# Optimization experiments

Hardware: AMD Instinct MI355X
Metric: run time of the kernel (lower is better)

The kernel has to match this reference:

```python
import jax, jax.numpy as jnp
import numpy as np

N_NODES = 50000
N_EDGES = 800000
N_FEAT = 128
D_HID = 128
N_CLASS = 40


def gcn_conv(x, W, b, src, dst, n_nodes):
    """PyG GCNConv: h = D^{-1/2} (A + I) D^{-1/2} (x @ W) + b.
    src/dst are int arrays [E]; self-loops handled analytically."""
    h = x @ W  # [N, D]
    ones = jnp.ones(src.shape[0], dtype=h.dtype)
    # degree after adding self-loops: 1 + in-degree (edge weights are 1)
    deg = 1.0 + jax.ops.segment_sum(ones, dst, num_segments=n_nodes)
    dinv = jax.lax.rsqrt(deg)  # [N]
    # messages along edges src -> dst with symmetric normalization
    msg = h[src] * (dinv[src] * dinv[dst])[:, None]  # [E, D]
    agg = jax.ops.segment_sum(msg, dst, num_segments=n_nodes)  # [N, D]
    # self-loop contribution: dinv[i]^2 * h[i]
    agg = agg + h * (dinv * dinv)[:, None]
    return agg + b


def setup_inputs() -> dict:
    key = jax.random.key(0)
    ks = jax.random.split(key, 5)
    x = jax.random.normal(ks[0], (N_NODES, N_FEAT), dtype=jnp.float32)
    edge_index = jax.random.randint(ks[1], (2, N_EDGES), 0, N_NODES, dtype=jnp.int64)
    s_in = 1.0 / np.sqrt(N_FEAT)
    s_h = 1.0 / np.sqrt(D_HID)
    W_in = jax.random.normal(ks[2], (N_FEAT, D_HID), dtype=jnp.float32) * s_in
    W1 = jax.random.normal(ks[3], (D_HID, D_HID), dtype=jnp.float32) * s_h
    W_out = jax.random.normal(ks[4], (D_HID, N_CLASS), dtype=jnp.float32) * s_h
    return {
        "x": x,
        "edge_index": edge_index,
        "W_in": W_in,
        "b_in": jnp.zeros((D_HID,), jnp.float32),
        "W1": W1,
        "b1": jnp.zeros((D_HID,), jnp.float32),
        "W_out": W_out,
        "b_out": jnp.zeros((N_CLASS,), jnp.float32),
    }


def reference(x, edge_index, W_in, b_in, W1, b1, W_out, b_out):
    src, dst = edge_index[0], edge_index[1]
    n = x.shape[0]
    # input GCNConv (no activation on input_fc, matching the torch forward)
    h = gcn_conv(x, W_in, b_in, src, dst, n)
    # hidden layer: dropout is identity at eval; relu after conv; normalize=False
    h = jax.nn.relu(gcn_conv(h, W1, b1, src, dst, n))
    out = h @ W_out + b_out
    return jax.nn.log_softmax(out, axis=1)
```

## Files before the change

### kernel.cpp

```cpp
#include <hip/hip_runtime.h>
#include <math.h>


#define THREADS 256

typedef __attribute__((ext_vector_type(8))) short short8v;
typedef __attribute__((ext_vector_type(4))) float float4v;

__device__ __forceinline__ float b2f(unsigned int lo16) {
    return __uint_as_float(lo16 << 16);
}
__device__ __forceinline__ unsigned short f2b(float f) {
    unsigned int u = __float_as_uint(f);
    u += 0x7FFFu + ((u >> 16) & 1u);
    return (unsigned short)(u >> 16);
}

__global__ void detect_idx64(const int* __restrict__ idx, int* __restrict__ flag) {
    int t = threadIdx.x;
    unsigned long long b = __ballot(idx[2 * t + 1] == 0);
    if (t == 0) *flag = (b == 0xFFFFFFFFFFFFFFFFull) ? 1 : 0;
}

__global__ void fill_pos(const int* __restrict__ idx, const int* __restrict__ flag,
                         int* __restrict__ cnt, unsigned int* __restrict__ rec, int E) {
    int e = blockIdx.x * blockDim.x + threadIdx.x;
    if (e >= E) return;
    int f = *flag;
    int src, dst;
    if (f) { src = idx[2 * e]; dst = idx[2 * (E + e)]; }
    else   { src = idx[e];     dst = idx[E + e]; }
    unsigned int pos = (unsigned int)atomicAdd(&cnt[dst], 1);
    rec[e] = ((unsigned int)src << 16) | (pos & 0xFFFFu);
}

__global__ __launch_bounds__(256) void scanA(const int* __restrict__ cnt,
                                             int* __restrict__ bsum, int N) {
    __shared__ int wt[4];
    int tid = threadIdx.x, lane = tid & 63, w = tid >> 6;
    int i = blockIdx.x * 256 + tid;
    int v = (i < N) ? cnt[i] : 0;
    int s = v;
#pragma unroll
    for (int off = 1; off < 64; off <<= 1) {
        int t = __shfl_up(s, off);
        if (lane >= off) s += t;
    }
    if (lane == 63) wt[w] = s;
    __syncthreads();
    if (tid == 0) bsum[blockIdx.x] = wt[0] + wt[1] + wt[2] + wt[3];
}

__global__ __launch_bounds__(256) void scanB(int* __restrict__ bsum,
                                             int* __restrict__ boff,
                                             int* __restrict__ rowstart,
                                             int nb, int N) {
    __shared__ int wt[4];
    __shared__ int wo[5];
    int tid = threadIdx.x, lane = tid & 63, w = tid >> 6;
    int v = (tid < nb) ? bsum[tid] : 0;
    int s = v;
#pragma unroll
    for (int off = 1; off < 64; off <<= 1) {
        int t = __shfl_up(s, off);
        if (lane >= off) s += t;
    }
    if (lane == 63) wt[w] = s;
    __syncthreads();
    if (tid == 0) {
        int run = 0;
#pragma unroll
        for (int k = 0; k < 4; ++k) { wo[k] = run; run += wt[k]; }
        wo[4] = run;
    }
    __syncthreads();
    if (tid < nb) boff[tid] = wo[w] + s - v;
    if (tid == 0) rowstart[N] = wo[4];
}

__global__ __launch_bounds__(256) void scanC(const int* __restrict__ cnt,
                                             const int* __restrict__ boff,
                                             int* __restrict__ rowstart,
                                             float* __restrict__ dinv, int N) {
    __shared__ int wt[4];
    __shared__ int wo[4];
    int tid = threadIdx.x, lane = tid & 63, w = tid >> 6;
    int i = blockIdx.x * 256 + tid;
    int v = (i < N) ? cnt[i] : 0;
    int s = v;
#pragma unroll
    for (int off = 1; off < 64; off <<= 1) {
        int t = __shfl_up(s, off);
        if (lane >= off) s += t;
    }
    if (lane == 63) wt[w] = s;
    __syncthreads();
    if (tid == 0) {
        int run = 0;
#pragma unroll
        for (int k = 0; k < 4; ++k) { wo[k] = run; run += wt[k]; }
    }
    __syncthreads();
    if (i < N) {
        rowstart[i] = boff[blockIdx.x] + wo[w] + (s - v);
        dinv[i] = rsqrtf(1.0f + (float)v);
    }
}

__global__ void fill_place(const int* __restrict__ idx, const int* __restrict__ flag,
                           const unsigned int* __restrict__ rec,
                           const int* __restrict__ rowstart,
                           unsigned short* __restrict__ srcs, int E) {
    int e = blockIdx.x * blockDim.x + threadIdx.x;
    if (e >= E) return;
    int f = *flag;
    int dst = f ? idx[2 * (E + e)] : idx[E + e];
    unsigned int r = rec[e];
    srcs[rowstart[dst] + (int)(r & 0xFFFFu)] = (unsigned short)(r >> 16);
}

__global__ __launch_bounds__(256) void pack_w(const float* __restrict__ W,
                                              uint4* __restrict__ wpk) {
    int tid = threadIdx.x;
    for (int it = 0; it < 8; ++it) {
        int s = it * 256 + tid;
        int ct = s >> 8;
        int kb = (s >> 6) & 3;
        int l  = s & 63;
        int col = ct * 16 + (l & 15);
        int k0  = kb * 32 + ((l >> 4) << 3);
        unsigned short e0 = f2b(W[(k0 + 0) * 128 + col]);
        unsigned short e1 = f2b(W[(k0 + 1) * 128 + col]);
        unsigned short e2 = f2b(W[(k0 + 2) * 128 + col]);
        unsigned short e3 = f2b(W[(k0 + 3) * 128 + col]);
        unsigned short e4 = f2b(W[(k0 + 4) * 128 + col]);
        unsigned short e5 = f2b(W[(k0 + 5) * 128 + col]);
        unsigned short e6 = f2b(W[(k0 + 6) * 128 + col]);
        unsigned short e7 = f2b(W[(k0 + 7) * 128 + col]);
        uint4 u;
        u.x = (unsigned int)e0 | ((unsigned int)e1 << 16);
        u.y = (unsigned int)e2 | ((unsigned int)e3 << 16);
        u.z = (unsigned int)e4 | ((unsigned int)e5 << 16);
        u.w = (unsigned int)e6 | ((unsigned int)e7 << 16);
        wpk[s] = u;
    }
}

template <int ABF>
__global__ __launch_bounds__(256) void gemm_mfma(const void* __restrict__ Ap,
                                                 const uint4* __restrict__ wpk,
                                                 unsigned short* __restrict__ outb,
                                                 int N) {
    __shared__ unsigned short ol[64 * 128];
    int tid = threadIdx.x;
    int w = tid >> 6, l = tid & 63;
    int lr = l & 15, lq = l >> 4;
    int row0 = blockIdx.x * 64 + w * 16;
    int arow = row0 + lr;
    int arow_c = (arow < N) ? arow : (N > 0 ? N - 1 : 0);

    float4v acc[8];
#pragma unroll
    for (int ct = 0; ct < 8; ++ct) acc[ct] = (float4v){0.f, 0.f, 0.f, 0.f};

#pragma unroll
    for (int kb = 0; kb < 4; ++kb) {
        short8v af;
        if (ABF) {
            uint4 v = *(const uint4*)((const unsigned short*)Ap + (size_t)arow_c * 128 + kb * 32 + lq * 8);
            union { uint4 u; short8v s; } cv; cv.u = v; af = cv.s;
        } else {
            const float* ap = (const float*)Ap + (size_t)arow_c * 128 + kb * 32 + lq * 8;
            float4 va = *(const float4*)ap;
            float4 vb = *(const float4*)(ap + 4);
            uint4 u;
            u.x = (unsigned int)f2b(va.x) | ((unsigned int)f2b(va.y) << 16);
            u.y = (unsigned int)f2b(va.z) | ((unsigned int)f2b(va.w) << 16);
            u.z = (unsigned int)f2b(vb.x) | ((unsigned int)f2b(vb.y) << 16);
            u.w = (unsigned int)f2b(vb.z) | ((unsigned int)f2b(vb.w) << 16);
            union { uint4 uu; short8v s; } cv; cv.uu = u; af = cv.s;
        }
#pragma unroll
        for (int ct = 0; ct < 8; ++ct) {
            uint4 bv = wpk[(ct * 4 + kb) * 64 + l];
            union { uint4 u; short8v s; } cv; cv.u = bv; short8v bf = cv.s;
            acc[ct] = __builtin_amdgcn_mfma_f32_16x16x32_bf16(af, bf, acc[ct], 0, 0, 0);
        }
    }

#pragma unroll
    for (int ct = 0; ct < 8; ++ct) {
#pragma unroll
        for (int r = 0; r < 4; ++r) {
            int dr = lq * 4 + r;
            ol[(w * 16 + dr) * 128 + ct * 16 + lr] = f2b(acc[ct][r]);
        }
    }
    __syncthreads();
#pragma unroll
    for (int it = 0; it < 4; ++it) {
        int o = it * 4096 + tid * 16;
        int rr = o >> 8;
        int cb = o & 255;
        int gr = blockIdx.x * 64 + rr;
        if (gr < N) {
            uint4 v = *(const uint4*)((const char*)ol + o);
            *(uint4*)((char*)outb + (size_t)gr * 256 + cb) = v;
        }
    }
}

__global__ __launch_bounds__(256) void agg_node(const unsigned short* __restrict__ hb,
                                                const int* __restrict__ rowstart,
                                                const unsigned short* __restrict__ srcs,
                                                const float* __restrict__ dinv,
                                                const float* __restrict__ b,
                                                unsigned short* __restrict__ outb,
                                                int N, int do_relu) {
    int w = threadIdx.x >> 6, lane = threadIdx.x & 63;
    int node = blockIdx.x * 4 + w;
    if (node >= N) return;
    int beg = rowstart[node], end = rowstart[node + 1];
    float dn = dinv[node];
    int quarter = lane >> 4, q = lane & 15;
    const uint4* hb8 = (const uint4*)hb;
    float a0 = 0.f, a1 = 0.f, a2 = 0.f, a3 = 0.f;
    float a4 = 0.f, a5 = 0.f, a6 = 0.f, a7 = 0.f;

    for (int j0 = beg; j0 < end; j0 += 64) {
        int myj = j0 + lane;
        int ms = 0;
        float md = 0.f;
        if (myj < end) { ms = (int)srcs[myj]; md = dinv[ms]; }
        int m = min(64, end - j0);
#pragma unroll 2
        for (int k = 0; k < m; k += 4) {
            int idx2 = k + quarter;
            int s = __shfl(ms, idx2);
            float c = dn * __shfl(md, idx2);
            uint4 v = hb8[(size_t)s * 16 + q];
            a0 += c * b2f(v.x & 0xFFFFu);
            a1 += c * b2f(v.x >> 16);
            a2 += c * b2f(v.y & 0xFFFFu);
            a3 += c * b2f(v.y >> 16);
            a4 += c * b2f(v.z & 0xFFFFu);
            a5 += c * b2f(v.z >> 16);
            a6 += c * b2f(v.w & 0xFFFFu);
            a7 += c * b2f(v.w >> 16);
        }
    }
    a0 += __shfl_xor(a0, 32); a1 += __shfl_xor(a1, 32);
    a2 += __shfl_xor(a2, 32); a3 += __shfl_xor(a3, 32);
    a4 += __shfl_xor(a4, 32); a5 += __shfl_xor(a5, 32);
    a6 += __shfl_xor(a6, 32); a7 += __shfl_xor(a7, 32);
    a0 += __shfl_xor(a0, 16); a1 += __shfl_xor(a1, 16);
    a2 += __shfl_xor(a2, 16); a3 += __shfl_xor(a3, 16);
    a4 += __shfl_xor(a4, 16); a5 += __shfl_xor(a5, 16);
    a6 += __shfl_xor(a6, 16); a7 += __shfl_xor(a7, 16);

    if (quarter == 0) {
        uint4 sv = hb8[(size_t)node * 16 + q];
        float d2 = dn * dn;
        float4 b0 = ((const float4*)b)[2 * q];
        float4 b1 = ((const float4*)b)[2 * q + 1];
        float r0 = a0 + d2 * b2f(sv.x & 0xFFFFu) + b0.x;
        float r1 = a1 + d2 * b2f(sv.x >> 16)     + b0.y;
        float r2 = a2 + d2 * b2f(sv.y & 0xFFFFu) + b0.z;
        float r3 = a3 + d2 * b2f(sv.y >> 16)     + b0.w;
        float r4 = a4 + d2 * b2f(sv.z & 0xFFFFu) + b1.x;
        float r5 = a5 + d2 * b2f(sv.z >> 16)     + b1.y;
        float r6 = a6 + d2 * b2f(sv.w & 0xFFFFu) + b1.z;
        float r7 = a7 + d2 * b2f(sv.w >> 16)     + b1.w;
        if (do_relu) {
            r0 = fmaxf(r0, 0.f); r1 = fmaxf(r1, 0.f);
            r2 = fmaxf(r2, 0.f); r3 = fmaxf(r3, 0.f);
            r4 = fmaxf(r4, 0.f); r5 = fmaxf(r5, 0.f);
            r6 = fmaxf(r6, 0.f); r7 = fmaxf(r7, 0.f);
        }
        uint4 o;
        o.x = (unsigned int)f2b(r0) | ((unsigned int)f2b(r1) << 16);
        o.y = (unsigned int)f2b(r2) | ((unsigned int)f2b(r3) << 16);
        o.z = (unsigned int)f2b(r4) | ((unsigned int)f2b(r5) << 16);
        o.w = (unsigned int)f2b(r6) | ((unsigned int)f2b(r7) << 16);
        ((uint4*)outb)[(size_t)node * 16 + q] = o;
    }
}

__global__ __launch_bounds__(256) void out_gemm(const unsigned short* __restrict__ h2b,
                                                const float* __restrict__ Wout,
                                                const float* __restrict__ bout,
                                                float* __restrict__ out, int N) {
    __shared__ float Xt[128 * 128];
    __shared__ float Wl[128 * 40];
    __shared__ float bl[40];
    int tid = threadIdx.x;
    int row0 = blockIdx.x * 128;

    for (int i = tid; i < 128 * 40; i += 256) Wl[i] = Wout[i];
    if (tid < 40) bl[tid] = bout[tid];

    {
        int r = tid >> 1, kh = tid & 1;
        int gr = row0 + r;
#pragma unroll
        for (int i = 0; i < 16; ++i) {
            int k = kh * 64 + i * 4;
            float f0, f1, f2, f3;
            if (gr < N) {
                uint2 qv = ((const uint2*)h2b)[(size_t)gr * 32 + (k >> 2)];
                f0 = b2f(qv.x & 0xFFFFu); f1 = b2f(qv.x >> 16);
                f2 = b2f(qv.y & 0xFFFFu); f3 = b2f(qv.y >> 16);
            } else {
                f0 = f1 = f2 = f3 = 0.f;
            }
            Xt[(k + 0) * 128 + r] = f0;
            Xt[(k + 1) * 128 + r] = f1;
            Xt[(k + 2) * 128 + r] = f2;
            Xt[(k + 3) * 128 + r] = f3;
        }
    }
    __syncthreads();

    int cg = tid & 7;
    int r4 = tid >> 3;
    float bias[5];
#pragma unroll
    for (int c = 0; c < 5; ++c) bias[c] = bl[5 * cg + c];

    float acc[4][5];
#pragma unroll
    for (int j = 0; j < 4; ++j)
#pragma unroll
        for (int c = 0; c < 5; ++c) acc[j][c] = 0.f;

    const float4* Xt4 = (const float4*)Xt;
#pragma unroll 4
    for (int k = 0; k < 128; ++k) {
        float4 xv = Xt4[k * 32 + r4];
        const float* wr = &Wl[k * 40 + 5 * cg];
        float w0 = wr[0], w1 = wr[1], w2 = wr[2], w3 = wr[3], w4 = wr[4];
        float xs[4] = {xv.x, xv.y, xv.z, xv.w};
#pragma unroll
        for (int j = 0; j < 4; ++j) {
            acc[j][0] += xs[j] * w0;
            acc[j][1] += xs[j] * w1;
            acc[j][2] += xs[j] * w2;
            acc[j][3] += xs[j] * w3;
            acc[j][4] += xs[j] * w4;
        }
    }

#pragma unroll
    for (int j = 0; j < 4; ++j) {
        int r = row0 + r4 * 4 + j;
        if (r >= N) continue;
        float v[5];
        float m = -INFINITY;
#pragma unroll
        for (int c = 0; c < 5; ++c) { v[c] = acc[j][c] + bias[c]; m = fmaxf(m, v[c]); }
        m = fmaxf(m, __shfl_xor(m, 1));
        m = fmaxf(m, __shfl_xor(m, 2));
        m = fmaxf(m, __shfl_xor(m, 4));
        float s = 0.f;
#pragma unroll
        for (int c = 0; c < 5; ++c) s += expf(v[c] - m);
        s += __shfl_xor(s, 1);
        s += __shfl_xor(s, 2);
        s += __shfl_xor(s, 4);
        float ls = logf(s);
#pragma unroll
        for (int c = 0; c < 5; ++c) out[(size_t)r * 40 + 5 * cg + c] = v[c] - m - ls;
    }
}

static inline size_t al256(size_t x) { return (x + 255) & ~(size_t)255; }

extern "C" void kernel_launch(void* const* d_in, const int* in_sizes, int n_in,
                              void* d_out, int out_size, void* d_ws, size_t ws_size,
                              hipStream_t stream) {
    const float* x     = (const float*)d_in[0];
    const int*   idx   = (const int*)d_in[1];
    const float* W_in  = (const float*)d_in[2];
    const float* b_in  = (const float*)d_in[3];
    const float* W1    = (const float*)d_in[4];
    const float* b1    = (const float*)d_in[5];
    const float* W_out = (const float*)d_in[6];
    const float* b_out = (const float*)d_in[7];
    float* out = (float*)d_out;

    int N = in_sizes[0] / 128;
    int E = in_sizes[1] / 2;

    char* ws = (char*)d_ws;
    size_t off = 0;
    int* flag = (int*)(ws + off);              off += 256;
    int* cnt = (int*)(ws + off);               off += al256((size_t)N * 4);
    int* rowstart = (int*)(ws + off);          off += al256((size_t)(N + 1) * 4);
    float* dinv = (float*)(ws + off);          off += al256((size_t)N * 4);
    unsigned short* srcs = (unsigned short*)(ws + off); off += al256((size_t)E * 2);
    unsigned int* rec = (unsigned int*)(ws + off);      off += al256((size_t)E * 4);
    int* bsum = (int*)(ws + off);              off += 2048;
    int* boff = (int*)(ws + off);              off += 2048;
    uint4* wpk1 = (uint4*)(ws + off);          off += 32768;
    uint4* wpk2 = (uint4*)(ws + off);          off += 32768;
    unsigned short* B0 = (unsigned short*)(ws + off);   off += (size_t)N * 128 * 2;
    unsigned short* B1 = (unsigned short*)(ws + off);

    int nb_e = (E + THREADS - 1) / THREADS;
    int nb_n = (N + THREADS - 1) / THREADS;
    int nb_g = (N + 63) / 64;
    int nb_o = (N + 127) / 128;
    int nb_a = (N + 3) / 4;

    detect_idx64<<<1, 64, 0, stream>>>(idx, flag);
    hipMemsetAsync(cnt, 0, (size_t)N * 4, stream);
    pack_w<<<1, THREADS, 0, stream>>>(W_in, wpk1);
    pack_w<<<1, THREADS, 0, stream>>>(W1, wpk2);
    fill_pos<<<nb_e, THREADS, 0, stream>>>(idx, flag, cnt, rec, E);
    scanA<<<nb_n, THREADS, 0, stream>>>(cnt, bsum, N);
    scanB<<<1, THREADS, 0, stream>>>(bsum, boff, rowstart, nb_n, N);
    scanC<<<nb_n, THREADS, 0, stream>>>(cnt, boff, rowstart, dinv, N);
    fill_place<<<nb_e, THREADS, 0, stream>>>(idx, flag, rec, rowstart, srcs, E);

    gemm_mfma<0><<<nb_g, THREADS, 0, stream>>>(x, wpk1, B0, N);
    agg_node<<<nb_a, THREADS, 0, stream>>>(B0, rowstart, srcs, dinv, b_in,
                                           B1, N, 0);
    gemm_mfma<1><<<nb_g, THREADS, 0, stream>>>(B1, wpk2, B0, N);
    agg_node<<<nb_a, THREADS, 0, stream>>>(B0, rowstart, srcs, dinv, b1,
                                           B1, N, 1);
    out_gemm<<<nb_o, THREADS, 0, stream>>>(B1, W_out, b_out, out, N);
}
```

Before: 263.4 us.

## Double GEMM row tile, unroll gather loop by two edges, merge weight packing

Each GEMM block now computes 128 rows instead of 64, so every weight fragment load feeds two MFMAs. The goal is to halve weight traffic per output and launch fewer blocks. The aggregation inner loop now handles eight edges per iteration with two independent gathers in flight, which adds memory-level parallelism. The two weight-pack launches become one two-block launch. In exchange there are more registers for accumulators, a doubled LDS tile, and potentially lower occupancy.

```diff
diff --git a/kernel.cpp b/kernel.cpp
--- a/kernel.cpp
+++ b/kernel.cpp
@@ -119,8 +119,12 @@
     srcs[rowstart[dst] + (int)(r & 0xFFFFu)] = (unsigned short)(r >> 16);
 }
 
-__global__ __launch_bounds__(256) void pack_w(const float* __restrict__ W,
-                                              uint4* __restrict__ wpk) {
+__global__ __launch_bounds__(256) void pack_w2(const float* __restrict__ W0,
+                                               const float* __restrict__ W1,
+                                               uint4* __restrict__ wpk0,
+                                               uint4* __restrict__ wpk1) {
+    const float* W = blockIdx.x ? W1 : W0;
+    uint4* wpk = blockIdx.x ? wpk1 : wpk0;
     int tid = threadIdx.x;
     for (int it = 0; it < 8; ++it) {
         int s = it * 256 + tid;
@@ -151,58 +155,70 @@
                                                  const uint4* __restrict__ wpk,
                                                  unsigned short* __restrict__ outb,
                                                  int N) {
-    __shared__ unsigned short ol[64 * 128];
+    __shared__ unsigned short ol[128 * 128];
     int tid = threadIdx.x;
     int w = tid >> 6, l = tid & 63;
     int lr = l & 15, lq = l >> 4;
-    int row0 = blockIdx.x * 64 + w * 16;
-    int arow = row0 + lr;
-    int arow_c = (arow < N) ? arow : (N > 0 ? N - 1 : 0);
-
-    float4v acc[8];
-#pragma unroll
-    for (int ct = 0; ct < 8; ++ct) acc[ct] = (float4v){0.f, 0.f, 0.f, 0.f};
+    int base = blockIdx.x * 128;
+    int arow0 = base + w * 16 + lr;
+    int arow1 = base + 64 + w * 16 + lr;
+    int ar0 = (arow0 < N) ? arow0 : (N - 1);
+    int ar1 = (arow1 < N) ? arow1 : (N - 1);
+
+    float4v acc[2][8];
+#pragma unroll
+    for (int t = 0; t < 2; ++t)
+#pragma unroll
+        for (int ct = 0; ct < 8; ++ct) acc[t][ct] = (float4v){0.f, 0.f, 0.f, 0.f};
 
 #pragma unroll
     for (int kb = 0; kb < 4; ++kb) {
-        short8v af;
+        short8v af0, af1;
         if (ABF) {
-            uint4 v = *(const uint4*)((const unsigned short*)Ap + (size_t)arow_c * 128 + kb * 32 + lq * 8);
-            union { uint4 u; short8v s; } cv; cv.u = v; af = cv.s;
+            uint4 v0 = *(const uint4*)((const unsigned short*)Ap + (size_t)ar0 * 128 + kb * 32 + lq * 8);
+            uint4 v1 = *(const uint4*)((const unsigned short*)Ap + (size_t)ar1 * 128 + kb * 32 + lq * 8);
+            union { uint4 u; short8v s; } c0, c1; c0.u = v0; c1.u = v1;
+            af0 = c0.s; af1 = c1.s;
         } else {
-            const float* ap = (const float*)Ap + (size_t)arow_c * 128 + kb * 32 + lq * 8;
-            float4 va = *(const float4*)ap;
-            float4 vb = *(const float4*)(ap + 4);
-            uint4 u;
-            u.x = (unsigned int)f2b(va.x) | ((unsigned int)f2b(va.y) << 16);
-            u.y = (unsigned int)f2b(va.z) | ((unsigned int)f2b(va.w) << 16);
-            u.z = (unsigned int)f2b(vb.x) | ((unsigned int)f2b(vb.y) << 16);
-            u.w = (unsigned int)f2b(vb.z) | ((unsigned int)f2b(vb.w) << 16);
-            union { uint4 uu; short8v s; } cv; cv.uu = u; af = cv.s;
+            const float* a0 = (const float*)Ap + (size_t)ar0 * 128 + kb * 32 + lq * 8;
+            const float* a1 = (const float*)Ap + (size_t)ar1 * 128 + kb * 32 + lq * 8;
+            float4 va0 = *(const float4*)a0, vb0 = *(const float4*)(a0 + 4);
+            float4 va1 = *(const float4*)a1, vb1 = *(const float4*)(a1 + 4);
+            uint4 u0, u1;
+            u0.x = (unsigned int)f2b(va0.x) | ((unsigned int)f2b(va0.y) << 16);
+            u0.y = (unsigned int)f2b(va0.z) | ((unsigned int)f2b(va0.w) << 16);
+            u0.z = (unsigned int)f2b(vb0.x) | ((unsigned int)f2b(vb0.y) << 16);
+            u0.w = (unsigned int)f2b(vb0.z) | ((unsigned int)f2b(vb0.w) << 16);
+            u1.x = (unsigned int)f2b(va1.x) | ((unsigned int)f2b(va1.y) << 16);
+            u1.y = (unsigned int)f2b(va1.z) | ((unsigned int)f2b(va1.w) << 16);
+            u1.z = (unsigned int)f2b(vb1.x) | ((unsigned int)f2b(vb1.y) << 16);
+            u1.w = (unsigned int)f2b(vb1.z) | ((unsigned int)f2b(vb1.w) << 16);
+            union { uint4 uu; short8v s; } c0, c1; c0.uu = u0; c1.uu = u1;
+            af0 = c0.s; af1 = c1.s;
         }
 #pragma unroll
         for (int ct = 0; ct < 8; ++ct) {
             uint4 bv = wpk[(ct * 4 + kb) * 64 + l];
             union { uint4 u; short8v s; } cv; cv.u = bv; short8v bf = cv.s;
-            acc[ct] = __builtin_amdgcn_mfma_f32_16x16x32_bf16(af, bf, acc[ct], 0, 0, 0);
-        }
-    }
-
-#pragma unroll
-    for (int ct = 0; ct < 8; ++ct) {
-#pragma unroll
-        for (int r = 0; r < 4; ++r) {
-            int dr = lq * 4 + r;
-            ol[(w * 16 + dr) * 128 + ct * 16 + lr] = f2b(acc[ct][r]);
-        }
-    }
-    __syncthreads();
-#pragma unroll
-    for (int it = 0; it < 4; ++it) {
+            acc[0][ct] = __builtin_amdgcn_mfma_f32_16x16x32_bf16(af0, bf, acc[0][ct], 0, 0, 0);
+            acc[1][ct] = __builtin_amdgcn_mfma_f32_16x16x32_bf16(af1, bf, acc[1][ct], 0, 0, 0);
+        }
+    }
+
+#pragma unroll
+    for (int t = 0; t < 2; ++t)
+#pragma unroll
+        for (int ct = 0; ct < 8; ++ct)
+#pragma unroll
+            for (int r = 0; r < 4; ++r)
+                ol[(t * 64 + w * 16 + lq * 4 + r) * 128 + ct * 16 + lr] = f2b(acc[t][ct][r]);
+    __syncthreads();
+#pragma unroll
+    for (int it = 0; it < 8; ++it) {
         int o = it * 4096 + tid * 16;
         int rr = o >> 8;
         int cb = o & 255;
-        int gr = blockIdx.x * 64 + rr;
+        int gr = base + rr;
         if (gr < N) {
             uint4 v = *(const uint4*)((const char*)ol + o);
             *(uint4*)((char*)outb + (size_t)gr * 256 + cb) = v;
@@ -234,19 +250,31 @@
         if (myj < end) { ms = (int)srcs[myj]; md = dinv[ms]; }
         int m = min(64, end - j0);
 #pragma unroll 2
-        for (int k = 0; k < m; k += 4) {
-            int idx2 = k + quarter;
-            int s = __shfl(ms, idx2);
-            float c = dn * __shfl(md, idx2);
-            uint4 v = hb8[(size_t)s * 16 + q];
-            a0 += c * b2f(v.x & 0xFFFFu);
-            a1 += c * b2f(v.x >> 16);
-            a2 += c * b2f(v.y & 0xFFFFu);
-            a3 += c * b2f(v.y >> 16);
-            a4 += c * b2f(v.z & 0xFFFFu);
-            a5 += c * b2f(v.z >> 16);
-            a6 += c * b2f(v.w & 0xFFFFu);
-            a7 += c * b2f(v.w >> 16);
+        for (int k = 0; k < m; k += 8) {
+            int i0 = k + quarter;
+            int i1 = k + 4 + quarter;
+            int s0 = __shfl(ms, i0);
+            int s1 = __shfl(ms, i1);
+            float c0 = dn * __shfl(md, i0);
+            float c1 = dn * __shfl(md, i1);
+            uint4 v0 = hb8[(size_t)s0 * 16 + q];
+            uint4 v1 = hb8[(size_t)s1 * 16 + q];
+            a0 += c0 * b2f(v0.x & 0xFFFFu);
+            a1 += c0 * b2f(v0.x >> 16);
+            a2 += c0 * b2f(v0.y & 0xFFFFu);
+            a3 += c0 * b2f(v0.y >> 16);
+            a4 += c0 * b2f(v0.z & 0xFFFFu);
+            a5 += c0 * b2f(v0.z >> 16);
+            a6 += c0 * b2f(v0.w & 0xFFFFu);
+            a7 += c0 * b2f(v0.w >> 16);
+            a0 += c1 * b2f(v1.x & 0xFFFFu);
+            a1 += c1 * b2f(v1.x >> 16);
+            a2 += c1 * b2f(v1.y & 0xFFFFu);
+            a3 += c1 * b2f(v1.y >> 16);
+            a4 += c1 * b2f(v1.z & 0xFFFFu);
+            a5 += c1 * b2f(v1.z >> 16);
+            a6 += c1 * b2f(v1.w & 0xFFFFu);
+            a7 += c1 * b2f(v1.w >> 16);
         }
     }
     a0 += __shfl_xor(a0, 32); a1 += __shfl_xor(a1, 32);
@@ -408,14 +436,12 @@
 
     int nb_e = (E + THREADS - 1) / THREADS;
     int nb_n = (N + THREADS - 1) / THREADS;
-    int nb_g = (N + 63) / 64;
-    int nb_o = (N + 127) / 128;
+    int nb_g = (N + 127) / 128;
     int nb_a = (N + 3) / 4;
 
     detect_idx64<<<1, 64, 0, stream>>>(idx, flag);
     hipMemsetAsync(cnt, 0, (size_t)N * 4, stream);
-    pack_w<<<1, THREADS, 0, stream>>>(W_in, wpk1);
-    pack_w<<<1, THREADS, 0, stream>>>(W1, wpk2);
+    pack_w2<<<2, THREADS, 0, stream>>>(W_in, W1, wpk1, wpk2);
     fill_pos<<<nb_e, THREADS, 0, stream>>>(idx, flag, cnt, rec, E);
     scanA<<<nb_n, THREADS, 0, stream>>>(cnt, bsum, N);
     scanB<<<1, THREADS, 0, stream>>>(bsum, boff, rowstart, nb_n, N);
@@ -428,5 +454,5 @@
     gemm_mfma<1><<<nb_g, THREADS, 0, stream>>>(B1, wpk2, B0, N);
     agg_node<<<nb_a, THREADS, 0, stream>>>(B0, rowstart, srcs, dinv, b1,
                                            B1, N, 1);
-    out_gemm<<<nb_o, THREADS, 0, stream>>>(B1, W_out, b_out, out, N);
-}
+    out_gemm<<<nb_g, THREADS, 0, stream>>>(B1, W_out, b_out, out, N);
+}
```

Result: no change. 260.6 us (-1.1%).
